# Kernel optimization log

Measured on AMD Instinct MI355X. Metric: run time of the kernel, lower is better.

The kernel has to match this reference:

```python
import jax, jax.numpy as jnp
import numpy as np

UNITS = 20
EPS_GPE_STN = 0.1


def _w_lateral(units=UNITS, eps=EPS_GPE_STN):
    # Faithful port of generate_distance_matrix: grid_size = int(sqrt(units))
    grid_size = int(units ** 0.5)
    idx = np.arange(units)
    xi, yi = np.divmod(idx, grid_size)
    d = (xi[:, None] - xi[None, :]) ** 2 + (yi[:, None] - yi[None, :]) ** 2
    return jnp.asarray(np.exp(-d.astype(np.float32) / eps), dtype=jnp.float32)


def setup_inputs() -> dict:
    key = jax.random.key(0)
    ks = jax.random.split(key, 8)
    B = 524288
    k = 1.0 / np.sqrt(UNITS)  # PyTorch LSTMCell init scale
    x = jax.random.normal(ks[0], (B, UNITS), dtype=jnp.float32)
    h = jax.random.normal(ks[1], (B, UNITS), dtype=jnp.float32)
    c = jax.random.normal(ks[2], (B, UNITS), dtype=jnp.float32)
    W_ih = jax.random.uniform(ks[3], (4 * UNITS, UNITS), jnp.float32, -k, k)
    W_hh = jax.random.uniform(ks[4], (4 * UNITS, UNITS), jnp.float32, -k, k)
    b_ih = jax.random.uniform(ks[5], (4 * UNITS,), jnp.float32, -k, k)
    b_hh = jax.random.uniform(ks[6], (4 * UNITS,), jnp.float32, -k, k)
    W_lat = _w_lateral()
    return {"x": x, "h": h, "c": c, "W_ih": W_ih, "W_hh": W_hh,
            "b_ih": b_ih, "b_hh": b_hh, "W_lat": W_lat}


def reference(x, h, c, W_ih, W_hh, b_ih, b_hh, W_lat):
    # nn.LSTMCell: gates in (i, f, g, o) order
    gates = x @ W_ih.T + h @ W_hh.T + (b_ih + b_hh)  # [B, 4U]
    i, f, g, o = jnp.split(gates, 4, axis=-1)
    c_next = jax.nn.sigmoid(f) * c + jax.nn.sigmoid(i) * jnp.tanh(g)
    h_lstm = jax.nn.sigmoid(o) * jnp.tanh(c_next)
    # bmm(W_lateral, h[:, :, None]).squeeze(-1) == h @ W_lat.T, then tanh
    h_next = jnp.tanh(h_lstm @ W_lat.T)
    return (h_next, c_next)
```

## Files before the change

kernel.cpp:

```cpp
#include <hip/hip_runtime.h>

#define UNITS 20

typedef __attribute__((ext_vector_type(8))) short short8;
typedef __attribute__((ext_vector_type(4))) float floatx4;
typedef __attribute__((ext_vector_type(4))) unsigned int u32x4;
typedef unsigned int u32;
typedef unsigned short u16;

__device__ __forceinline__ float rcpf_fast(float x) { return __builtin_amdgcn_rcpf(x); }
__device__ __forceinline__ float sigmoidf_fast(float x) { return rcpf_fast(1.0f + __expf(-x)); }
__device__ __forceinline__ float tanhf_fast(float x) { return 1.0f - 2.0f * rcpf_fast(1.0f + __expf(2.0f * x)); }

__device__ __forceinline__ u32 f2bf(float f) {
  u32 u = __builtin_bit_cast(u32, f);
  u += 0x7fffu + ((u >> 16) & 1u);
  return u >> 16;
}
__device__ __forceinline__ u32 cvtpk(float lo, float hi) {
  u32 r;
  asm("v_cvt_pk_bf16_f32 %0, %1, %2" : "=v"(r) : "v"(lo), "v"(hi));
  return r;
}

__global__ void prep_kernel(const float* __restrict__ W_ih, const float* __restrict__ W_hh,
                            const float* __restrict__ b_ih, const float* __restrict__ b_hh,
                            const float* __restrict__ W_lat,
                            u16* __restrict__ fragsG, u16* __restrict__ fragsL,
                            float4* __restrict__ bias4) {
  int tid = threadIdx.x;
  for (int e = tid; e < 768; e += 256) {
    int fi = e >> 6, lane = e & 63;
    int r = lane & 15, q = lane >> 4;
    short8 v8;
    if (fi < 10) {
      int t = fi >> 1, cc = fi & 1;
      int gr = (r & 3) * 20 + (r >> 2) * 5 + t;
#pragma unroll
      for (int j = 0; j < 8; ++j) {
        int k = cc * 32 + q * 8 + j;
        float v = 0.0f;
        if (k < 20) v = W_ih[gr * UNITS + k];
        else if (k < 40) v = W_hh[gr * UNITS + (k - 20)];
        v8[j] = (short)f2bf(v);
      }
      *(short8*)(fragsG + (size_t)e * 8) = v8;
    } else {
      int t = fi - 10;
      int vr = t * 16 + r;
#pragma unroll
      for (int j = 0; j < 8; ++j) {
        float v = (vr < 20 && j < 5) ? W_lat[vr * UNITS + q * 5 + j] : 0.0f;
        v8[j] = (short)f2bf(v);
      }
      *(short8*)(fragsL + (size_t)(t * 64 + lane) * 8) = v8;
    }
  }
  if (tid < 20)
    bias4[tid] = make_float4(b_ih[tid] + b_hh[tid],
                             b_ih[20 + tid] + b_hh[20 + tid],
                             b_ih[40 + tid] + b_hh[40 + tid],
                             b_ih[60 + tid] + b_hh[60 + tid]);
}

__global__ __launch_bounds__(256) void stn_main(
    const float* __restrict__ x, const float* __restrict__ h, const float* __restrict__ c,
    const u16* __restrict__ fragsG, const u16* __restrict__ fragsL,
    const float4* __restrict__ bias4, float* __restrict__ out, int B) {
  __shared__ float4 ldsGf[640];

  {
    const float4* src = (const float4*)fragsG;
    for (int i = threadIdx.x; i < 640; i += 256) ldsGf[i] = src[i];
  }

  const int tid  = threadIdx.x;
  const int lane = tid & 63;
  const int wv   = tid >> 6;
  const int m = lane & 15, q = lane >> 4;

  floatx4 biasr[5];
#pragma unroll
  for (int t = 0; t < 5; ++t) {
    float4 b4 = bias4[q * 5 + t];
    biasr[t] = (floatx4){b4.x, b4.y, b4.z, b4.w};
  }
  short8 afL0 = *(const short8*)(fragsL + (size_t)(0 * 64 + lane) * 8);
  short8 afL1 = *(const short8*)(fragsL + (size_t)(1 * 64 + lane) * 8);

  __syncthreads();

  const short8* aG = (const short8*)ldsGf;
  const float4* x4 = (const float4*)x;
  const float4* h4 = (const float4*)h;
  float* outh = out;
  float* outc = out + (size_t)B * UNITS;

  const long stride = 64L * (long)gridDim.x;
  for (long base = (long)blockIdx.x * 64; base < B; base += stride) {
    long row = base + wv * 16 + m;
    bool valid = row < (long)B;
    long rl  = valid ? row : (long)B - 1;
    long r5  = rl * 5;
    long r20 = rl * 20;

    float4 v0 = (q == 3) ? h4[r5 + 1] : x4[r5 + 2 * q];
    float4 v1 = (q == 0) ? x4[r5 + 1]
              : (q == 1) ? x4[r5 + 3]
              : (q == 2) ? h4[r5 + 0] : h4[r5 + 2];
    const float* cp = c + r20 + q * 5;
    float cv0 = cp[0], cv1 = cp[1], cv2 = cp[2], cv3 = cp[3], cv4 = cp[4];
    short8 bfr1 = {0, 0, 0, 0, 0, 0, 0, 0};
    if (q == 0) {
      float4 v2 = h4[r5 + 3];
      float4 v3 = h4[r5 + 4];
      u32x4 p1 = {cvtpk(v2.x, v2.y), cvtpk(v2.z, v2.w),
                  cvtpk(v3.x, v3.y), cvtpk(v3.z, v3.w)};
      bfr1 = __builtin_bit_cast(short8, p1);
    }
    u32x4 p0 = {cvtpk(v0.x, v0.y), cvtpk(v0.z, v0.w),
                cvtpk(v1.x, v1.y), cvtpk(v1.z, v1.w)};
    short8 bfr0 = __builtin_bit_cast(short8, p0);

    floatx4 acc[5];
#pragma unroll
    for (int t = 0; t < 5; ++t) {
      acc[t] = __builtin_amdgcn_mfma_f32_16x16x32_bf16(aG[(t * 2 + 0) * 64 + lane], bfr0, biasr[t], 0, 0, 0);
      acc[t] = __builtin_amdgcn_mfma_f32_16x16x32_bf16(aG[(t * 2 + 1) * 64 + lane], bfr1, acc[t], 0, 0, 0);
    }

    float cvv[5] = {cv0, cv1, cv2, cv3, cv4};
    float cn[5], hl[5];
#pragma unroll
    for (int t = 0; t < 5; ++t) {
      float ig = sigmoidf_fast(acc[t][0]);
      float fg = sigmoidf_fast(acc[t][1]);
      float gg = tanhf_fast(acc[t][2]);
      float og = sigmoidf_fast(acc[t][3]);
      float cnv = fg * cvv[t] + ig * gg;
      cn[t] = cnv;
      hl[t] = og * tanhf_fast(cnv);
    }

    u32x4 pl = {cvtpk(hl[0], hl[1]), cvtpk(hl[2], hl[3]), cvtpk(hl[4], 0.0f), 0u};
    short8 bl = __builtin_bit_cast(short8, pl);
    floatx4 z4 = {0.0f, 0.0f, 0.0f, 0.0f};
    floatx4 accL0 = __builtin_amdgcn_mfma_f32_16x16x32_bf16(afL0, bl, z4, 0, 0, 0);
    floatx4 accL1 = __builtin_amdgcn_mfma_f32_16x16x32_bf16(afL1, bl, z4, 0, 0, 0);

    if (valid) {
      float* co = outc + r20 + q * 5;
      co[0] = cn[0]; co[1] = cn[1]; co[2] = cn[2]; co[3] = cn[3]; co[4] = cn[4];
      float4 hv;
      hv.x = tanhf_fast(accL0[0]); hv.y = tanhf_fast(accL0[1]);
      hv.z = tanhf_fast(accL0[2]); hv.w = tanhf_fast(accL0[3]);
      *(float4*)(outh + r20 + q * 4) = hv;
      if (q == 0) {
        float4 hw;
        hw.x = tanhf_fast(accL1[0]); hw.y = tanhf_fast(accL1[1]);
        hw.z = tanhf_fast(accL1[2]); hw.w = tanhf_fast(accL1[3]);
        *(float4*)(outh + r20 + 16) = hw;
      }
    }
  }
}

extern "C" void kernel_launch(void* const* d_in, const int* in_sizes, int n_in,
                              void* d_out, int out_size, void* d_ws, size_t ws_size,
                              hipStream_t stream) {
  const float* x     = (const float*)d_in[0];
  const float* h     = (const float*)d_in[1];
  const float* c     = (const float*)d_in[2];
  const float* W_ih  = (const float*)d_in[3];
  const float* W_hh  = (const float*)d_in[4];
  const float* b_ih  = (const float*)d_in[5];
  const float* b_hh  = (const float*)d_in[6];
  const float* W_lat = (const float*)d_in[7];
  float* out = (float*)d_out;

  u16*    fragsG = (u16*)d_ws;
  u16*    fragsL = (u16*)((char*)d_ws + 10240);
  float4* bias4  = (float4*)((char*)d_ws + 12288);

  int B = in_sizes[0] / UNITS;
  prep_kernel<<<1, 256, 0, stream>>>(W_ih, W_hh, b_ih, b_hh, W_lat, fragsG, fragsL, bias4);
  long chunks = ((long)B + 63) / 64;
  int grid = (int)(chunks < 2048 ? chunks : 2048);
  stn_main<<<grid, 256, 0, stream>>>(x, h, c, fragsG, fragsL, bias4, out, B);
}
```

Before: 205.1 us.

## Coalesce row loads via LDS staging and prefetch next tile's inputs

Each wave now loads its 16 rows of x, h and c as contiguous float4 blocks across lanes, converts x and h to bf16 into a per-wave LDS scratch, and reads the MFMA B-fragments and c values back from LDS. This replaces the old scattered per-lane gathers. The next iteration's global loads are issued before the current MFMA and activation work so that memory latency overlaps with compute. The tail is handled by clamping the row base so duplicate rows are rewritten instead of masked, and launch bounds now request 4 blocks per CU. The costs are more LDS use, extra LDS round trips, and more live registers.

Measured after the change: 203.4 us. No clear change (-0.9%).

```diff
diff --git a/kernel.cpp b/kernel.cpp
--- a/kernel.cpp
+++ b/kernel.cpp
@@ -4,6 +4,7 @@
 
 typedef __attribute__((ext_vector_type(8))) short short8;
 typedef __attribute__((ext_vector_type(4))) float floatx4;
+typedef __attribute__((ext_vector_type(2))) unsigned int u32x2;
 typedef __attribute__((ext_vector_type(4))) unsigned int u32x4;
 typedef unsigned int u32;
 typedef unsigned short u16;
@@ -63,64 +64,102 @@
                              b_ih[60 + tid] + b_hh[60 + tid]);
 }
 
-__global__ __launch_bounds__(256) void stn_main(
+__global__ __launch_bounds__(256, 4) void stn_main(
     const float* __restrict__ x, const float* __restrict__ h, const float* __restrict__ c,
     const u16* __restrict__ fragsG, const u16* __restrict__ fragsL,
     const float4* __restrict__ bias4, float* __restrict__ out, int B) {
-  __shared__ float4 ldsGf[640];
-
-  {
-    const float4* src = (const float4*)fragsG;
-    for (int i = threadIdx.x; i < 640; i += 256) ldsGf[i] = src[i];
-  }
+  __shared__ unsigned char smem[20480];
+
+  for (int i = threadIdx.x; i < 640; i += 256)
+    ((float4*)smem)[i] = ((const float4*)fragsG)[i];
 
   const int tid  = threadIdx.x;
   const int lane = tid & 63;
   const int wv   = tid >> 6;
   const int m = lane & 15, q = lane >> 4;
 
+  unsigned char* Zb = smem + 10240 + wv * 2560;
+  float*         Cw = (float*)(Zb + 1280);
+
+  const int m0 = lane / 5, j0 = lane - m0 * 5;
+  const int l1 = 64 + lane;
+  const int m1 = l1 / 5, j1 = l1 - m1 * 5;
+  const int zA = m0 * 80 + 8 * j0;
+  const int zB = m1 * 80 + 8 * j1;
+
   floatx4 biasr[5];
 #pragma unroll
   for (int t = 0; t < 5; ++t) {
     float4 b4 = bias4[q * 5 + t];
     biasr[t] = (floatx4){b4.x, b4.y, b4.z, b4.w};
   }
-  short8 afL0 = *(const short8*)(fragsL + (size_t)(0 * 64 + lane) * 8);
-  short8 afL1 = *(const short8*)(fragsL + (size_t)(1 * 64 + lane) * 8);
+  short8 afL0 = *(const short8*)(fragsL + (size_t)lane * 8);
+  short8 afL1 = *(const short8*)(fragsL + (size_t)(64 + lane) * 8);
 
   __syncthreads();
 
-  const short8* aG = (const short8*)ldsGf;
-  const float4* x4 = (const float4*)x;
-  const float4* h4 = (const float4*)h;
+  const short8* aG = (const short8*)smem;
   float* outh = out;
   float* outc = out + (size_t)B * UNITS;
 
   const long stride = 64L * (long)gridDim.x;
-  for (long base = (long)blockIdx.x * 64; base < B; base += stride) {
-    long row = base + wv * 16 + m;
-    bool valid = row < (long)B;
-    long rl  = valid ? row : (long)B - 1;
-    long r5  = rl * 5;
-    long r20 = rl * 20;
-
-    float4 v0 = (q == 3) ? h4[r5 + 1] : x4[r5 + 2 * q];
-    float4 v1 = (q == 0) ? x4[r5 + 1]
-              : (q == 1) ? x4[r5 + 3]
-              : (q == 2) ? h4[r5 + 0] : h4[r5 + 2];
-    const float* cp = c + r20 + q * 5;
-    float cv0 = cp[0], cv1 = cp[1], cv2 = cp[2], cv3 = cp[3], cv4 = cp[4];
-    short8 bfr1 = {0, 0, 0, 0, 0, 0, 0, 0};
-    if (q == 0) {
-      float4 v2 = h4[r5 + 3];
-      float4 v3 = h4[r5 + 4];
-      u32x4 p1 = {cvtpk(v2.x, v2.y), cvtpk(v2.z, v2.w),
-                  cvtpk(v3.x, v3.y), cvtpk(v3.z, v3.w)};
-      bfr1 = __builtin_bit_cast(short8, p1);
-    }
-    u32x4 p0 = {cvtpk(v0.x, v0.y), cvtpk(v0.z, v0.w),
-                cvtpk(v1.x, v1.y), cvtpk(v1.z, v1.w)};
-    short8 bfr0 = __builtin_bit_cast(short8, p0);
+  long base = (long)blockIdx.x * 64;
+
+  auto rbclamp = [&](long b) {
+    long r = b + wv * 16;
+    if (r + 16 > (long)B) r = (long)B - 16;
+    if (r < 0) r = 0;
+    return r;
+  };
+
+  float4 xA, hA, cA;
+  float4 xB = {0, 0, 0, 0}, hB = {0, 0, 0, 0}, cB = {0, 0, 0, 0};
+
+  long rb = rbclamp(base);
+  {
+    const float4* xp = (const float4*)(x + rb * 20);
+    const float4* hp = (const float4*)(h + rb * 20);
+    const float4* cp = (const float4*)(c + rb * 20);
+    xA = xp[lane]; hA = hp[lane]; cA = cp[lane];
+    if (lane < 16) { xB = xp[64 + lane]; hB = hp[64 + lane]; cB = cp[64 + lane]; }
+  }
+
+  while (true) {
+    {
+      u32x2 w;
+      w[0] = cvtpk(xA.x, xA.y); w[1] = cvtpk(xA.z, xA.w);
+      *(u32x2*)(Zb + zA) = w;
+      w[0] = cvtpk(hA.x, hA.y); w[1] = cvtpk(hA.z, hA.w);
+      *(u32x2*)(Zb + zA + 40) = w;
+      *(float4*)((unsigned char*)Cw + lane * 16) = cA;
+      if (lane < 16) {
+        w[0] = cvtpk(xB.x, xB.y); w[1] = cvtpk(xB.z, xB.w);
+        *(u32x2*)(Zb + zB) = w;
+        w[0] = cvtpk(hB.x, hB.y); w[1] = cvtpk(hB.z, hB.w);
+        *(u32x2*)(Zb + zB + 40) = w;
+        *(float4*)((unsigned char*)Cw + 1024 + lane * 16) = cB;
+      }
+    }
+
+    long nbase = base + stride;
+    bool more = nbase < (long)B;
+
+    short8 bfr0 = *(const short8*)(Zb + m * 80 + q * 16);
+    short8 bfr1 = (short8){0, 0, 0, 0, 0, 0, 0, 0};
+    if (q == 0) bfr1 = *(const short8*)(Zb + m * 80 + 64);
+    float cvv[5];
+#pragma unroll
+    for (int t = 0; t < 5; ++t) cvv[t] = Cw[m * 20 + q * 5 + t];
+
+    long rbn = rb;
+    if (more) {
+      rbn = rbclamp(nbase);
+      const float4* xp = (const float4*)(x + rbn * 20);
+      const float4* hp = (const float4*)(h + rbn * 20);
+      const float4* cp = (const float4*)(c + rbn * 20);
+      xA = xp[lane]; hA = hp[lane]; cA = cp[lane];
+      if (lane < 16) { xB = xp[64 + lane]; hB = hp[64 + lane]; cB = cp[64 + lane]; }
+    }
 
     floatx4 acc[5];
 #pragma unroll
@@ -129,7 +168,6 @@
       acc[t] = __builtin_amdgcn_mfma_f32_16x16x32_bf16(aG[(t * 2 + 1) * 64 + lane], bfr1, acc[t], 0, 0, 0);
     }
 
-    float cvv[5] = {cv0, cv1, cv2, cv3, cv4};
     float cn[5], hl[5];
 #pragma unroll
     for (int t = 0; t < 5; ++t) {
@@ -148,7 +186,8 @@
     floatx4 accL0 = __builtin_amdgcn_mfma_f32_16x16x32_bf16(afL0, bl, z4, 0, 0, 0);
     floatx4 accL1 = __builtin_amdgcn_mfma_f32_16x16x32_bf16(afL1, bl, z4, 0, 0, 0);
 
-    if (valid) {
+    {
+      long r20 = (rb + m) * 20;
       float* co = outc + r20 + q * 5;
       co[0] = cn[0]; co[1] = cn[1]; co[2] = cn[2]; co[3] = cn[3]; co[4] = cn[4];
       float4 hv;
@@ -162,6 +201,9 @@
         *(float4*)(outh + r20 + 16) = hw;
       }
     }
+
+    if (!more) break;
+    base = nbase; rb = rbn;
   }
 }
 
```

## Triple-buffer x/h tiles into LDS via async global_load_lds pipeline

Applied to the files above, without the earlier changes.

Replaces direct per-lane global loads of x and h with asynchronous global_load_lds copies into a per-wave triple-buffered LDS ring, prefetching two iterations ahead and waiting with explicit vmcnt counts. The c values are register double-buffered one iteration ahead, the loop is manually unrolled via macros, and the grid is reduced to 768 blocks with launch_bounds(256,2). The aim is to hide HBM latency in this memory-bound kernel, at the cost of 40KB of LDS per block, lower occupancy, and fragile hand-tuned waitcnt values. Tail handling now clamps rows rather than masking, so the last chunk rewrites overlapping rows with identical values.

Result: no change. 207.5 us (+1.1%).

```diff
diff --git a/kernel.cpp b/kernel.cpp
--- a/kernel.cpp
+++ b/kernel.cpp
@@ -21,6 +21,15 @@
   u32 r;
   asm("v_cvt_pk_bf16_f32 %0, %1, %2" : "=v"(r) : "v"(lo), "v"(hi));
   return r;
+}
+
+typedef __attribute__((address_space(1))) unsigned char u8_g;
+typedef __attribute__((address_space(3))) unsigned char u8_l;
+__device__ __forceinline__ void gl_lds16(const float* g, unsigned char* s) {
+  __builtin_amdgcn_global_load_lds((const u8_g*)(const void*)g, (u8_l*)(void*)s, 16, 0, 0);
+}
+__device__ __forceinline__ void gl_lds4(const float* g, unsigned char* s) {
+  __builtin_amdgcn_global_load_lds((const u8_g*)(const void*)g, (u8_l*)(void*)s, 4, 0, 0);
 }
 
 __global__ void prep_kernel(const float* __restrict__ W_ih, const float* __restrict__ W_hh,
@@ -63,106 +72,141 @@
                              b_ih[60 + tid] + b_hh[60 + tid]);
 }
 
-__global__ __launch_bounds__(256) void stn_main(
+__global__ __launch_bounds__(256, 2) void stn_main(
     const float* __restrict__ x, const float* __restrict__ h, const float* __restrict__ c,
     const u16* __restrict__ fragsG, const u16* __restrict__ fragsL,
     const float4* __restrict__ bias4, float* __restrict__ out, int B) {
-  __shared__ float4 ldsGf[640];
-
-  {
-    const float4* src = (const float4*)fragsG;
-    for (int i = threadIdx.x; i < 640; i += 256) ldsGf[i] = src[i];
-  }
+  __shared__ unsigned char smem[40960];
+
+  for (int i = threadIdx.x; i < 640; i += 256)
+    ((float4*)smem)[i] = ((const float4*)fragsG)[i];
 
   const int tid  = threadIdx.x;
   const int lane = tid & 63;
   const int wv   = tid >> 6;
   const int m = lane & 15, q = lane >> 4;
 
+  unsigned char* SBASE = smem + 10240 + wv * 7680;
+
   floatx4 biasr[5];
 #pragma unroll
   for (int t = 0; t < 5; ++t) {
     float4 b4 = bias4[q * 5 + t];
     biasr[t] = (floatx4){b4.x, b4.y, b4.z, b4.w};
   }
-  short8 afL0 = *(const short8*)(fragsL + (size_t)(0 * 64 + lane) * 8);
-  short8 afL1 = *(const short8*)(fragsL + (size_t)(1 * 64 + lane) * 8);
+  short8 afL0 = *(const short8*)(fragsL + (size_t)lane * 8);
+  short8 afL1 = *(const short8*)(fragsL + (size_t)(64 + lane) * 8);
 
   __syncthreads();
 
-  const short8* aG = (const short8*)ldsGf;
-  const float4* x4 = (const float4*)x;
-  const float4* h4 = (const float4*)h;
+  const short8* aG = (const short8*)smem;
   float* outh = out;
   float* outc = out + (size_t)B * UNITS;
 
   const long stride = 64L * (long)gridDim.x;
-  for (long base = (long)blockIdx.x * 64; base < B; base += stride) {
-    long row = base + wv * 16 + m;
-    bool valid = row < (long)B;
-    long rl  = valid ? row : (long)B - 1;
-    long r5  = rl * 5;
-    long r20 = rl * 20;
-
-    float4 v0 = (q == 3) ? h4[r5 + 1] : x4[r5 + 2 * q];
-    float4 v1 = (q == 0) ? x4[r5 + 1]
-              : (q == 1) ? x4[r5 + 3]
-              : (q == 2) ? h4[r5 + 0] : h4[r5 + 2];
-    const float* cp = c + r20 + q * 5;
-    float cv0 = cp[0], cv1 = cp[1], cv2 = cp[2], cv3 = cp[3], cv4 = cp[4];
-    short8 bfr1 = {0, 0, 0, 0, 0, 0, 0, 0};
-    if (q == 0) {
-      float4 v2 = h4[r5 + 3];
-      float4 v3 = h4[r5 + 4];
-      u32x4 p1 = {cvtpk(v2.x, v2.y), cvtpk(v2.z, v2.w),
-                  cvtpk(v3.x, v3.y), cvtpk(v3.z, v3.w)};
-      bfr1 = __builtin_bit_cast(short8, p1);
+  long bA = (long)blockIdx.x * 64;
+
+  auto rbof = [&](long b) {
+    long r = b + wv * 16;
+    if (r + 16 > (long)B) r = (long)B - 16;
+    if (r < 0) r = 0;
+    return r;
+  };
+
+#define GL(SGL, bb) { \
+    long rb2_ = rbof(bb); \
+    const float* xs_ = x + rb2_ * 20; \
+    const float* hs_ = h + rb2_ * 20; \
+    unsigned char* d_ = SBASE + (SGL); \
+    gl_lds16(xs_ + lane * 4, d_); \
+    gl_lds4 (xs_ + 256 + lane, d_ + 1024); \
+    gl_lds16(hs_ + lane * 4, d_ + 1280); \
+    gl_lds4 (hs_ + 256 + lane, d_ + 2304); \
+  }
+
+#define PASS(SCUR, SGL, KW, CC, CF) { \
+    GL(SGL, bA + 2 * stride); \
+    asm volatile("s_waitcnt vmcnt(" KW ")" ::: "memory"); \
+    __builtin_amdgcn_sched_barrier(0); \
+    const unsigned char* X_ = SBASE + (SCUR); \
+    const unsigned char* H_ = X_ + 1280; \
+    const int mo_ = m * 80; \
+    const unsigned char* pA_ = (q == 0) ? X_ + mo_      : (q == 1) ? X_ + mo_ + 32 \
+                             : (q == 2) ? X_ + mo_ + 64 : H_ + mo_ + 16; \
+    const unsigned char* pB_ = (q == 0) ? X_ + mo_ + 16 : (q == 1) ? X_ + mo_ + 48 \
+                             : (q == 2) ? H_ + mo_      : H_ + mo_ + 32; \
+    float4 fa_ = *(const float4*)pA_; \
+    float4 fb_ = *(const float4*)pB_; \
+    u32x4 w0_ = {cvtpk(fa_.x, fa_.y), cvtpk(fa_.z, fa_.w), cvtpk(fb_.x, fb_.y), cvtpk(fb_.z, fb_.w)}; \
+    short8 bfr0 = __builtin_bit_cast(short8, w0_); \
+    short8 bfr1 = (short8){0, 0, 0, 0, 0, 0, 0, 0}; \
+    if (q == 0) { \
+      float4 ga_ = *(const float4*)(H_ + mo_ + 48); \
+      float4 gb_ = *(const float4*)(H_ + mo_ + 64); \
+      u32x4 w1_ = {cvtpk(ga_.x, ga_.y), cvtpk(ga_.z, ga_.w), cvtpk(gb_.x, gb_.y), cvtpk(gb_.z, gb_.w)}; \
+      bfr1 = __builtin_bit_cast(short8, w1_); \
+    } \
+    { long rb1_ = rbof(bA + stride); \
+      const float* cp_ = c + (rb1_ + m) * 20 + q * 5; \
+      _Pragma("unroll") for (int t = 0; t < 5; ++t) CF[t] = cp_[t]; } \
+    floatx4 acc[5]; \
+    _Pragma("unroll") for (int t = 0; t < 5; ++t) { \
+      acc[t] = __builtin_amdgcn_mfma_f32_16x16x32_bf16(aG[(t * 2 + 0) * 64 + lane], bfr0, biasr[t], 0, 0, 0); \
+      acc[t] = __builtin_amdgcn_mfma_f32_16x16x32_bf16(aG[(t * 2 + 1) * 64 + lane], bfr1, acc[t], 0, 0, 0); } \
+    float cn_[5], hl_[5]; \
+    _Pragma("unroll") for (int t = 0; t < 5; ++t) { \
+      float ig = sigmoidf_fast(acc[t][0]); \
+      float fg = sigmoidf_fast(acc[t][1]); \
+      float gg = tanhf_fast(acc[t][2]); \
+      float og = sigmoidf_fast(acc[t][3]); \
+      float cnv = fg * CC[t] + ig * gg; \
+      cn_[t] = cnv; hl_[t] = og * tanhf_fast(cnv); } \
+    u32x4 pl_ = {cvtpk(hl_[0], hl_[1]), cvtpk(hl_[2], hl_[3]), cvtpk(hl_[4], 0.0f), 0u}; \
+    short8 bl_ = __builtin_bit_cast(short8, pl_); \
+    floatx4 z4_ = {0.f, 0.f, 0.f, 0.f}; \
+    floatx4 aL0 = __builtin_amdgcn_mfma_f32_16x16x32_bf16(afL0, bl_, z4_, 0, 0, 0); \
+    floatx4 aL1 = __builtin_amdgcn_mfma_f32_16x16x32_bf16(afL1, bl_, z4_, 0, 0, 0); \
+    { long r20_ = (rbof(bA) + m) * 20; \
+      float* co_ = outc + r20_ + q * 5; \
+      co_[0] = cn_[0]; co_[1] = cn_[1]; co_[2] = cn_[2]; co_[3] = cn_[3]; co_[4] = cn_[4]; \
+      float4 hv_; \
+      hv_.x = tanhf_fast(aL0[0]); hv_.y = tanhf_fast(aL0[1]); \
+      hv_.z = tanhf_fast(aL0[2]); hv_.w = tanhf_fast(aL0[3]); \
+      *(float4*)(outh + r20_ + q * 4) = hv_; \
+      if (q == 0) { \
+        float4 hw_; \
+        hw_.x = tanhf_fast(aL1[0]); hw_.y = tanhf_fast(aL1[1]); \
+        hw_.z = tanhf_fast(aL1[2]); hw_.w = tanhf_fast(aL1[3]); \
+        *(float4*)(outh + r20_ + 16) = hw_; } } \
+    bool more_ = (bA + stride) < (long)B; \
+    bA += stride; \
+    if (!more_) break; \
+  }
+
+  float cva[5], cvb[5];
+
+  GL(0, bA);
+  GL(2560, bA + stride);
+  { long rb0_ = rbof(bA);
+    const float* cp_ = c + (rb0_ + m) * 20 + q * 5;
+#pragma unroll
+    for (int t = 0; t < 5; ++t) cva[t] = cp_[t]; }
+
+  do {
+    PASS(0,    5120, "10", cva, cvb)
+    PASS(2560, 0,    "16", cvb, cva)
+    while (true) {
+      PASS(5120, 2560, "20", cva, cvb)
+      PASS(0,    5120, "20", cvb, cva)
+      PASS(2560, 0,    "20", cva, cvb)
+      PASS(5120, 2560, "20", cvb, cva)
+      PASS(0,    5120, "20", cva, cvb)
+      PASS(2560, 0,    "20", cvb, cva)
     }
-    u32x4 p0 = {cvtpk(v0.x, v0.y), cvtpk(v0.z, v0.w),
-                cvtpk(v1.x, v1.y), cvtpk(v1.z, v1.w)};
-    short8 bfr0 = __builtin_bit_cast(short8, p0);
-
-    floatx4 acc[5];
-#pragma unroll
-    for (int t = 0; t < 5; ++t) {
-      acc[t] = __builtin_amdgcn_mfma_f32_16x16x32_bf16(aG[(t * 2 + 0) * 64 + lane], bfr0, biasr[t], 0, 0, 0);
-      acc[t] = __builtin_amdgcn_mfma_f32_16x16x32_bf16(aG[(t * 2 + 1) * 64 + lane], bfr1, acc[t], 0, 0, 0);
-    }
-
-    float cvv[5] = {cv0, cv1, cv2, cv3, cv4};
-    float cn[5], hl[5];
-#pragma unroll
-    for (int t = 0; t < 5; ++t) {
-      float ig = sigmoidf_fast(acc[t][0]);
-      float fg = sigmoidf_fast(acc[t][1]);
-      float gg = tanhf_fast(acc[t][2]);
-      float og = sigmoidf_fast(acc[t][3]);
-      float cnv = fg * cvv[t] + ig * gg;
-      cn[t] = cnv;
-      hl[t] = og * tanhf_fast(cnv);
-    }
-
-    u32x4 pl = {cvtpk(hl[0], hl[1]), cvtpk(hl[2], hl[3]), cvtpk(hl[4], 0.0f), 0u};
-    short8 bl = __builtin_bit_cast(short8, pl);
-    floatx4 z4 = {0.0f, 0.0f, 0.0f, 0.0f};
-    floatx4 accL0 = __builtin_amdgcn_mfma_f32_16x16x32_bf16(afL0, bl, z4, 0, 0, 0);
-    floatx4 accL1 = __builtin_amdgcn_mfma_f32_16x16x32_bf16(afL1, bl, z4, 0, 0, 0);
-
-    if (valid) {
-      float* co = outc + r20 + q * 5;
-      co[0] = cn[0]; co[1] = cn[1]; co[2] = cn[2]; co[3] = cn[3]; co[4] = cn[4];
-      float4 hv;
-      hv.x = tanhf_fast(accL0[0]); hv.y = tanhf_fast(accL0[1]);
-      hv.z = tanhf_fast(accL0[2]); hv.w = tanhf_fast(accL0[3]);
-      *(float4*)(outh + r20 + q * 4) = hv;
-      if (q == 0) {
-        float4 hw;
-        hw.x = tanhf_fast(accL1[0]); hw.y = tanhf_fast(accL1[1]);
-        hw.z = tanhf_fast(accL1[2]); hw.w = tanhf_fast(accL1[3]);
-        *(float4*)(outh + r20 + 16) = hw;
-      }
-    }
-  }
+  } while (0);
+
+#undef PASS
+#undef GL
 }
 
 extern "C" void kernel_launch(void* const* d_in, const int* in_sizes, int n_in,
@@ -185,6 +229,6 @@
   int B = in_sizes[0] / UNITS;
   prep_kernel<<<1, 256, 0, stream>>>(W_ih, W_hh, b_ih, b_hh, W_lat, fragsG, fragsL, bias4);
   long chunks = ((long)B + 63) / 64;
-  int grid = (int)(chunks < 2048 ? chunks : 2048);
+  int grid = (int)(chunks < 768 ? chunks : 768);
   stn_main<<<grid, 256, 0, stream>>>(x, h, c, fragsG, fragsL, bias4, out, B);
 }
```
